# Performance work log

Hardware: AMD Instinct MI355X
Metric: run time of the kernel (lower is better)

## Reference

```python
import jax, jax.numpy as jnp
import numpy as np

B, T, E = 4, 2048, 2048
H, HKV, HD = 16, 8, 128
THETA = 10000.0
SCALE_BASE = 512.0


def _rotate_half(x):
    x1, x2 = jnp.split(x, 2, axis=-1)
    return jnp.concatenate([-x2, x1], axis=-1)


def _xpos_tables(seqlen):
    # cos/sin/scale tables for XPos rotary, all [seqlen, HD], fp32 compute dtype
    half_idx = jnp.arange(0, HD, 2, dtype=jnp.float32)
    inv_freq = 1.0 / (THETA ** (half_idx / HD))            # [HD/2]
    t = jnp.arange(seqlen, dtype=jnp.float32)
    freqs = jnp.outer(t, inv_freq)                          # [seqlen, HD/2]
    emb = jnp.concatenate([freqs, freqs], axis=-1)          # [seqlen, HD]
    cos, sin = jnp.cos(emb), jnp.sin(emb)
    # xpos decay: ((2i + 0.4d)/(1.4d)) ** ((t - L/2)/scale_base)
    scale_vec = (half_idx + 0.4 * HD) / (1.4 * HD)          # [HD/2]
    power = (t - seqlen // 2) / SCALE_BASE                  # [seqlen]
    scale = scale_vec[None, :] ** power[:, None]            # [seqlen, HD/2]
    scale = jnp.concatenate([scale, scale], axis=-1)        # [seqlen, HD]
    return cos, sin, scale


def setup_inputs() -> dict:
    key = jax.random.key(0)
    ks = jax.random.split(key, 5)
    std = 0.02
    return {
        "x": jax.random.normal(ks[0], (B, T, E), dtype=jnp.float32),
        "W_q": jax.random.normal(ks[1], (E, H * HD), dtype=jnp.float32) * std,
        "W_k": jax.random.normal(ks[2], (E, HKV * HD), dtype=jnp.float32) * std,
        "W_v": jax.random.normal(ks[3], (E, HKV * HD), dtype=jnp.float32) * std,
        "W_o": jax.random.normal(ks[4], (E, E), dtype=jnp.float32) * std,
    }


def reference(x, W_q, W_k, W_v, W_o):
    b, t, _ = x.shape
    q = (x @ W_q).reshape(b, t, H, HD)       # [B,T,H,HD]
    k = (x @ W_k).reshape(b, t, HKV, HD)     # [B,T,HKV,HD]
    v = (x @ W_v).reshape(b, t, HKV, HD)
    rep = H // HKV                            # GQA: repeat_interleave over head dim
    k = jnp.repeat(k, rep, axis=2)
    v = jnp.repeat(v, rep, axis=2)

    cos, sin, scale = _xpos_tables(t)         # past_len = 0 (no kv cache)
    cos = cos[None, :, None, :]
    sin = sin[None, :, None, :]
    scale = scale[None, :, None, :]
    q = q * scale
    q = q * cos + _rotate_half(q) * sin
    k = k / scale
    k = k * cos + _rotate_half(k) * sin

    inv_sqrt_d = 1.0 / jnp.sqrt(jnp.float32(HD))
    scores = jnp.einsum('bqhd,bkhd->bhqk', q, k) * inv_sqrt_d  # [B,H,T,T]
    causal = jnp.triu(jnp.ones((t, t), dtype=bool), k=1)
    scores = jnp.where(causal[None, None], -jnp.inf, scores)
    probs = jax.nn.softmax(scores, axis=-1)
    attn = jnp.einsum('bhqk,bkhd->bqhd', probs, v)             # [B,T,H,HD]
    out = attn.reshape(b, t, E) @ W_o
    return out
```

## Files before the change

kernel.cpp:

```cpp
#include <hip/hip_runtime.h>

typedef _Float16 f16;
typedef __attribute__((ext_vector_type(8))) _Float16 f16x8;
typedef __attribute__((ext_vector_type(4))) _Float16 f16x4;
typedef __attribute__((ext_vector_type(4))) float f32x4;
typedef __attribute__((ext_vector_type(16))) float f32x16;
typedef __attribute__((ext_vector_type(4))) unsigned u32x4;

#define T_SEQ 2048
#define NBATCH 4

__device__ __forceinline__ void gld_lds16(const f16* g, f16* l) {
    __builtin_amdgcn_global_load_lds((const __attribute__((address_space(1))) void*)g,
                                     (__attribute__((address_space(3))) void*)l, 16, 0, 0);
}

__device__ __forceinline__ unsigned pk2(float a, float b) {
    __attribute__((ext_vector_type(2))) __fp16 h = __builtin_amdgcn_cvt_pkrtz(a, b);
    return __builtin_bit_cast(unsigned, h);
}

__global__ __launch_bounds__(256) void k_prep(const float* __restrict__ x,
                                              const float* __restrict__ Wq,
                                              const float* __restrict__ Wk,
                                              const float* __restrict__ Wv,
                                              const float* __restrict__ Wo,
                                              f16* __restrict__ xh,
                                              f16* __restrict__ wqkvT,
                                              f16* __restrict__ woT,
                                              float* __restrict__ tab) {
    __shared__ float tile[32][33];
    int bidx = blockIdx.x;
    if (bidx < 16384) {
        int i = bidx * 256 + threadIdx.x;
        float4 v = ((const float4*)x)[i];
        f16x4 o = { (f16)v.x, (f16)v.y, (f16)v.z, (f16)v.w };
        ((f16x4*)xh)[i] = o;
        return;
    }
    bidx -= 16384;
    if (bidx >= 12288) {
        int i = (bidx - 12288) * 256 + threadIdx.x;
        int t = i >> 6, f = i & 63;
        float inv_freq = powf(10000.0f, -(2.0f * f) / 128.0f);
        float ang = (float)t * inv_freq;
        float sv = (2.0f * f + 51.2f) / 179.2f;
        float pw = ((float)t - 1024.0f) / 512.0f;
        tab[i] = cosf(ang);
        tab[131072 + i] = sinf(ang);
        tab[262144 + i] = powf(sv, pw);
        return;
    }
    const float* src; f16* dst; int N, bx, by;
    if (bidx < 4096)      { src = Wq; dst = wqkvT;                      N = 2048; bx = bidx & 63; by = bidx >> 6; }
    else if (bidx < 6144) { src = Wk; dst = wqkvT + (size_t)2048 * 2048; N = 1024; int t2 = bidx - 4096; bx = t2 & 31; by = t2 >> 5; }
    else if (bidx < 8192) { src = Wv; dst = wqkvT + (size_t)3072 * 2048; N = 1024; int t2 = bidx - 6144; bx = t2 & 31; by = t2 >> 5; }
    else                  { src = Wo; dst = woT;                        N = 2048; int t2 = bidx - 8192; bx = t2 & 63; by = t2 >> 6; }
    int n0 = bx * 32, k0 = by * 32;
    int tx = threadIdx.x & 31, ty = threadIdx.x >> 5;
#pragma unroll
    for (int j = 0; j < 32; j += 8)
        tile[ty + j][tx] = src[(size_t)(k0 + ty + j) * N + n0 + tx];
    __syncthreads();
#pragma unroll
    for (int j = 0; j < 32; j += 8)
        dst[(size_t)(n0 + ty + j) * 2048 + k0 + tx] = (f16)tile[tx][ty + j];
}

__global__ __launch_bounds__(256) void k_vtrans(const f16* __restrict__ qkv, f16* __restrict__ vtg) {
    const int kt = blockIdx.x, bk = blockIdx.y;
    const int b = bk >> 3, kvh = bk & 7;
    const int tid = threadIdx.x;
    __shared__ f16 tile[64][132];
#pragma unroll
    for (int p = 0; p < 4; ++p) {
        int idx = p * 256 + tid;
        int r = idx >> 4, dc = (idx & 15) * 8;
        f16x8 v = *(const f16x8*)(qkv + (size_t)(b * T_SEQ + kt * 64 + r) * 4096 + 3072 + kvh * 128 + dc);
#pragma unroll
        for (int j = 0; j < 8; ++j) tile[r][dc + j] = v[j];
    }
    __syncthreads();
    f16* outb = vtg + (size_t)(bk * 32 + kt) * 8192;
#pragma unroll
    for (int p = 0; p < 4; ++p) {
        int c = p * 256 + tid;
        int kchunk = c >> 7, d = c & 127;
        f16x8 o;
#pragma unroll
        for (int j = 0; j < 8; ++j) o[j] = tile[kchunk * 8 + j][d];
        *(f16x8*)(outb + (size_t)c * 8) = o;
    }
}

template <typename OutT>
__global__ __launch_bounds__(512, 1) void k_gemm256(const f16* __restrict__ A,
                                                    const f16* __restrict__ B,
                                                    OutT* __restrict__ C, int M, int N, int K) {
    extern __shared__ char smem[];
    f16* As = (f16*)smem;
    f16* Bs = (f16*)smem + 32768;
    const int tid = threadIdx.x, lane = tid & 63, w = tid >> 6;
    const int wr4 = w >> 1, wc2 = w & 1;
    const int cq = lane & 15, gq = lane >> 4;
    const int nbx = gridDim.x;
    const int bid0 = blockIdx.y * nbx + blockIdx.x;
    const int x = bid0 & 7, idx = bid0 >> 3;
    const int snb = (nbx == 16) ? 3 : 2;
    const int mt = (x >> 1) * 8 + (idx >> snb);
    const int nt = (x & 1) * (nbx >> 1) + (idx & ((nbx >> 1) - 1));
    const int m0 = mt * 256, n0 = nt * 256;
    const int KT = K >> 6;

    f32x4 acc[2][2][2][4] = {};
    f16x8 aL[2][2], aH[2][2], bL[4][2], bH[4][2];

    auto stageA = [&](int buf, int half, int t) {
#pragma unroll
        for (int r = 0; r < 2; ++r) {
            int cb = r * 512 + w * 64;
            int c = cb + lane;
            int row = c >> 3, cc = c & 7;
            gld_lds16(A + (size_t)(m0 + half * 128 + row) * K + t * 64 + ((cc ^ (row & 7)) * 8),
                      As + buf * 16384 + half * 8192 + cb * 8);
        }
    };
    auto stageB = [&](int buf, int half, int t) {
#pragma unroll
        for (int r = 0; r < 2; ++r) {
            int cb = r * 512 + w * 64;
            int c = cb + lane;
            int row = c >> 3, cc = c & 7;
            gld_lds16(B + (size_t)(n0 + half * 128 + row) * K + t * 64 + ((cc ^ (row & 7)) * 8),
                      Bs + buf * 16384 + half * 8192 + cb * 8);
        }
    };
    auto rdA = [&](int buf, int qr, f16x8 a[2][2]) {
#pragma unroll
        for (int mi = 0; mi < 2; ++mi)
#pragma unroll
            for (int ks = 0; ks < 2; ++ks) {
                int R = qr * 128 + wr4 * 32 + mi * 16 + cq;
                a[mi][ks] = *(const f16x8*)&As[buf * 16384 + R * 64 + (((ks * 4 + gq) ^ (cq & 7)) * 8)];
            }
    };
    auto rdB = [&](int buf, int qc, f16x8 b[4][2]) {
#pragma unroll
        for (int ni = 0; ni < 4; ++ni)
#pragma unroll
            for (int ks = 0; ks < 2; ++ks) {
                int R = qc * 128 + wc2 * 64 + ni * 16 + cq;
                b[ni][ks] = *(const f16x8*)&Bs[buf * 16384 + R * 64 + (((ks * 4 + gq) ^ (cq & 7)) * 8)];
            }
    };

    stageA(0, 0, 0); stageB(0, 0, 0); stageB(0, 1, 0); stageA(0, 1, 0);
    if (KT > 1) { stageA(1, 0, 1); stageB(1, 0, 1); stageB(1, 1, 1); }
    asm volatile("s_waitcnt vmcnt(6)");
    __builtin_amdgcn_s_barrier();

#pragma unroll 1
    for (int t = 0; t < KT; ++t) {
        const int buf = t & 1;
        rdA(buf, 0, aL); rdB(buf, 0, bL); rdB(buf, 1, bH); rdA(buf, 1, aH);
        __builtin_amdgcn_s_setprio(1);
#pragma unroll
        for (int mi = 0; mi < 2; ++mi)
#pragma unroll
            for (int ni = 0; ni < 4; ++ni)
#pragma unroll
                for (int ks = 0; ks < 2; ++ks)
                    acc[0][0][mi][ni] = __builtin_amdgcn_mfma_f32_16x16x32_f16(aL[mi][ks], bL[ni][ks], acc[0][0][mi][ni], 0, 0, 0);
        __builtin_amdgcn_s_setprio(0);
        if (t + 1 < KT) stageA(buf ^ 1, 1, t + 1);
        __builtin_amdgcn_s_setprio(1);
#pragma unroll
        for (int mi = 0; mi < 2; ++mi)
#pragma unroll
            for (int ni = 0; ni < 4; ++ni)
#pragma unroll
                for (int ks = 0; ks < 2; ++ks)
                    acc[0][1][mi][ni] = __builtin_amdgcn_mfma_f32_16x16x32_f16(aL[mi][ks], bH[ni][ks], acc[0][1][mi][ni], 0, 0, 0);
        __builtin_amdgcn_s_setprio(0);
        __builtin_amdgcn_s_barrier();
        if (t + 2 < KT) { stageA(buf, 0, t + 2); stageB(buf, 0, t + 2); stageB(buf, 1, t + 2); }
        __builtin_amdgcn_s_setprio(1);
#pragma unroll
        for (int mi = 0; mi < 2; ++mi)
#pragma unroll
            for (int ni = 0; ni < 4; ++ni)
#pragma unroll
                for (int ks = 0; ks < 2; ++ks)
                    acc[1][1][mi][ni] = __builtin_amdgcn_mfma_f32_16x16x32_f16(aH[mi][ks], bH[ni][ks], acc[1][1][mi][ni], 0, 0, 0);
#pragma unroll
        for (int mi = 0; mi < 2; ++mi)
#pragma unroll
            for (int ni = 0; ni < 4; ++ni)
#pragma unroll
                for (int ks = 0; ks < 2; ++ks)
                    acc[1][0][mi][ni] = __builtin_amdgcn_mfma_f32_16x16x32_f16(aH[mi][ks], bL[ni][ks], acc[1][0][mi][ni], 0, 0, 0);
        __builtin_amdgcn_s_setprio(0);
        if (t + 2 < KT)      asm volatile("s_waitcnt vmcnt(6)");
        else                 asm volatile("s_waitcnt vmcnt(0)");
        __builtin_amdgcn_s_barrier();
    }

#pragma unroll
    for (int qr = 0; qr < 2; ++qr)
#pragma unroll
        for (int qc = 0; qc < 2; ++qc)
#pragma unroll
            for (int mi = 0; mi < 2; ++mi)
#pragma unroll
                for (int ni = 0; ni < 4; ++ni)
#pragma unroll
                    for (int i = 0; i < 4; ++i) {
                        int row = m0 + qr * 128 + wr4 * 32 + mi * 16 + gq * 4 + i;
                        int col = n0 + qc * 128 + wc2 * 64 + ni * 16 + cq;
                        C[(size_t)row * N + col] = (OutT)acc[qr][qc][mi][ni][i];
                    }
}

__global__ __launch_bounds__(256) void k_rope(f16* __restrict__ qkv, const float* __restrict__ tab) {
    int idx = blockIdx.x * 256 + threadIdx.x;
    const int QTOT = NBATCH * T_SEQ * 16 * 64;
    int f, col0, bt;
    bool isQ = idx < QTOT;
    if (isQ) {
        f = idx & 63; int hh = (idx >> 6) & 15; bt = idx >> 10;
        col0 = hh * 128 + f;
    } else {
        int j = idx - QTOT;
        f = j & 63; int hh = (j >> 6) & 7; bt = j >> 9;
        col0 = 2048 + hh * 128 + f;
    }
    int t = bt & (T_SEQ - 1);
    float cs = tab[t * 64 + f], sn = tab[131072 + t * 64 + f], sc = tab[262144 + t * 64 + f];
    float mult = isQ ? sc * 0.08838834764831845f : 1.0f / sc;
    size_t p = (size_t)bt * 4096 + col0;
    float x1 = (float)qkv[p], x2 = (float)qkv[p + 64];
    qkv[p]      = (f16)((x1 * cs - x2 * sn) * mult);
    qkv[p + 64] = (f16)((x2 * cs + x1 * sn) * mult);
}

__global__ __launch_bounds__(512) void k_attn(const f16* __restrict__ qkv,
                                              const f16* __restrict__ vtg,
                                              f16* __restrict__ ao) {
    const int bid0 = blockIdx.x;
    const int bid = (bid0 & 7) * 32 + (bid0 >> 3);
    const int pr = bid & 7, kvh = (bid >> 3) & 7, b = bid >> 6;
    const int bk = b * 8 + kvh;
    const int tid = threadIdx.x, lane = tid & 63, w = tid >> 6;
    const int w4 = w & 3, hg = w >> 2;
    const int h = kvh * 2 + hg;
    const int l31 = lane & 31, hi = lane >> 5;

    __shared__ f16 Klds[2][64 * 128];
    __shared__ f16 Vlds[2][8 * 128 * 8];

    const f16* kbase = qkv + (size_t)b * T_SEQ * 4096 + 2048 + kvh * 128;
    const f16* vbase = vtg + (size_t)bk * 32 * 8192;

    auto stage = [&](int buf, int kt) {
#pragma unroll
        for (int qq = 0; qq < 2; ++qq) {
            int c = w * 128 + qq * 64 + lane;
            int row = c >> 4;
            int ch = (c & 15) ^ (row & 15);
            gld_lds16(kbase + (size_t)(kt * 64 + row) * 4096 + ch * 8,
                      &Klds[buf][(w * 128 + qq * 64) * 8]);
        }
#pragma unroll
        for (int qq = 0; qq < 2; ++qq) {
            int c = w * 128 + qq * 64 + lane;
            gld_lds16(vbase + ((size_t)kt * 1024 + c) * 8,
                      &Vlds[buf][(w * 128 + qq * 64) * 8]);
        }
    };

#pragma unroll 1
    for (int hf = 0; hf < 2; ++hf) {
        const int qt = hf ? pr : (15 - pr);
        const int q0 = qt * 128;
        const int nkt = 2 * qt + 2;
        const int qrow = q0 + w4 * 32 + l31;

        f16x8 qf[8];
#pragma unroll
        for (int ds = 0; ds < 8; ++ds)
            qf[ds] = *(const f16x8*)(qkv + (size_t)(b * T_SEQ + qrow) * 4096 + h * 128 + ds * 16 + hi * 8);

        f32x16 Ot[4] = {};
        float mrow = -1e30f, lrow = 0.0f;

        stage(0, 0);
        __syncthreads();

#pragma unroll 1
        for (int kt = 0; kt < nkt; ++kt) {
            const int kb = kt & 1;
            if (kt + 1 < nkt) stage(kb ^ 1, kt + 1);

            if (!(kt == 2 * qt + 1 && w4 < 2)) {
                f32x16 St0 = {}, St1 = {};
                __builtin_amdgcn_s_setprio(1);
#pragma unroll
                for (int ds = 0; ds < 8; ++ds) {
                    int slot = (((2 * ds + hi) ^ (l31 & 15)) << 3);
                    f16x8 k0 = *(const f16x8*)&Klds[kb][l31 * 128 + slot];
                    f16x8 k1 = *(const f16x8*)&Klds[kb][(32 + l31) * 128 + slot];
                    St0 = __builtin_amdgcn_mfma_f32_32x32x16_f16(k0, qf[ds], St0, 0, 0, 0);
                    St1 = __builtin_amdgcn_mfma_f32_32x32x16_f16(k1, qf[ds], St1, 0, 0, 0);
                }
                __builtin_amdgcn_s_setprio(0);

                if (kt >= 2 * qt) {
                    int kbase2 = kt * 64;
#pragma unroll
                    for (int r = 0; r < 16; ++r) {
                        int krel = (r & 3) + 8 * (r >> 2) + 4 * hi;
                        if (kbase2 + krel > qrow) St0[r] = -1e30f;
                        if (kbase2 + 32 + krel > qrow) St1[r] = -1e30f;
                    }
                }

                float tm[16];
#pragma unroll
                for (int r = 0; r < 16; ++r) tm[r] = fmaxf(St0[r], St1[r]);
#pragma unroll
                for (int d = 8; d >= 1; d >>= 1)
#pragma unroll
                    for (int r = 0; r < 8; ++r)
                        if (r < d) tm[r] = fmaxf(tm[r], tm[r + d]);
                float tmax = tm[0];
                float mtile = fmaxf(tmax, __shfl_xor(tmax, 32, 64));

                if (!__all((mtile - mrow) <= 8.0f)) {
                    float mnew = fmaxf(mrow, mtile);
                    float fs = __expf(mrow - mnew);
                    mrow = mnew;
                    lrow *= fs;
#pragma unroll
                    for (int dblk = 0; dblk < 4; ++dblk)
#pragma unroll
                        for (int e = 0; e < 16; ++e) Ot[dblk][e] *= fs;
                }
#pragma unroll
                for (int r = 0; r < 16; ++r) {
                    St0[r] = __expf(St0[r] - mrow);
                    St1[r] = __expf(St1[r] - mrow);
                }
                float ts[16];
#pragma unroll
                for (int r = 0; r < 16; ++r) ts[r] = St0[r] + St1[r];
#pragma unroll
                for (int d = 8; d >= 1; d >>= 1)
#pragma unroll
                    for (int r = 0; r < 8; ++r)
                        if (r < d) ts[r] += ts[r + d];
                float tsum = ts[0];
                lrow += tsum + __shfl_xor(tsum, 32, 64);

#define PV_P(o, pos) ((o) < 4 ? St0[((o) & 3) * 4 + (pos)] : St1[((o) & 3) * 4 + (pos)])
#pragma unroll
                for (int s = 0; s < 4; ++s) {
                    unsigned x1 = pk2(PV_P(2 * s, 0), PV_P(2 * s, 1));
                    unsigned x2 = pk2(PV_P(2 * s, 2), PV_P(2 * s, 3));
                    unsigned y1 = pk2(PV_P(2 * s + 1, 0), PV_P(2 * s + 1, 1));
                    unsigned y2 = pk2(PV_P(2 * s + 1, 2), PV_P(2 * s + 1, 3));
                    unsigned sx1 = __shfl_xor(x1, 32, 64);
                    unsigned sx2 = __shfl_xor(x2, 32, 64);
                    unsigned sy1 = __shfl_xor(y1, 32, 64);
                    unsigned sy2 = __shfl_xor(y2, 32, 64);
                    u32x4 pw;
                    pw[0] = hi ? sy1 : x1;
                    pw[1] = hi ? sy2 : x2;
                    pw[2] = hi ? y1 : sx1;
                    pw[3] = hi ? y2 : sx2;
                    f16x8 pa = __builtin_bit_cast(f16x8, pw);
                    __builtin_amdgcn_s_setprio(1);
#pragma unroll
                    for (int dblk = 0; dblk < 4; ++dblk) {
                        f16x8 vb = *(const f16x8*)&Vlds[kb][(((2 * s + hi) << 7) + 32 * dblk + l31) << 3];
                        Ot[dblk] = __builtin_amdgcn_mfma_f32_32x32x16_f16(vb, pa, Ot[dblk], 0, 0, 0);
                    }
                    __builtin_amdgcn_s_setprio(0);
                }
#undef PV_P
            }
            __syncthreads();
        }

        {
            float inv = 1.0f / lrow;
            size_t rowb = (size_t)(b * T_SEQ + qrow) * 2048 + h * 128;
#pragma unroll
            for (int dblk = 0; dblk < 4; ++dblk)
#pragma unroll
                for (int rg = 0; rg < 4; ++rg) {
                    f16x4 o4 = { (f16)(Ot[dblk][rg * 4 + 0] * inv), (f16)(Ot[dblk][rg * 4 + 1] * inv),
                                 (f16)(Ot[dblk][rg * 4 + 2] * inv), (f16)(Ot[dblk][rg * 4 + 3] * inv) };
                    *(f16x4*)(ao + rowb + dblk * 32 + rg * 8 + hi * 4) = o4;
                }
        }
    }
}

extern "C" void kernel_launch(void* const* d_in, const int* in_sizes, int n_in,
                              void* d_out, int out_size, void* d_ws, size_t ws_size,
                              hipStream_t stream) {
    const float* x  = (const float*)d_in[0];
    const float* Wq = (const float*)d_in[1];
    const float* Wk = (const float*)d_in[2];
    const float* Wv = (const float*)d_in[3];
    const float* Wo = (const float*)d_in[4];
    float* out = (float*)d_out;

    f16* xh    = (f16*)d_ws;
    f16* wqkvT = xh + (size_t)16777216;
    f16* woT   = wqkvT + (size_t)8388608;
    f16* qkv   = woT + (size_t)4194304;
    float* tab = (float*)(qkv + (size_t)33554432);
    f16* ao  = xh;
    f16* vtg = wqkvT;

    hipFuncSetAttribute(reinterpret_cast<const void*>(&k_gemm256<f16>),
                        hipFuncAttributeMaxDynamicSharedMemorySize, 131072);
    hipFuncSetAttribute(reinterpret_cast<const void*>(&k_gemm256<float>),
                        hipFuncAttributeMaxDynamicSharedMemorySize, 131072);

    k_prep<<<29184, 256, 0, stream>>>(x, Wq, Wk, Wv, Wo, xh, wqkvT, woT, tab);
    k_gemm256<f16><<<dim3(16, 32), 512, 131072, stream>>>(xh, wqkvT, qkv, 8192, 4096, 2048);
    k_vtrans<<<dim3(32, 32), 256, 0, stream>>>(qkv, vtg);
    k_rope<<<49152, 256, 0, stream>>>(qkv, tab);
    k_attn<<<256, 512, 0, stream>>>(qkv, vtg, ao);
    k_gemm256<float><<<dim3(8, 32), 512, 131072, stream>>>(ao, woT, out, 8192, 2048, 2048);
}
```

Before: 373.7 us.

## Triple-buffer K/V tiles in attention with explicit vmcnt waits

Moves the attention kernel's K/V shared buffers to dynamic LDS with three stages instead of two. Loads are issued two tiles ahead, and each iteration waits with a counted s_waitcnt vmcnt plus a raw s_barrier instead of a full __syncthreads. This is meant to hide more global-load latency behind the MFMA work. In exchange it uses 96KB of LDS and depends on hand-counted outstanding loads (4 per stage), which is fragile if the compiler emits other vector memory ops inside the loop.

```diff
diff --git a/kernel.cpp b/kernel.cpp
--- a/kernel.cpp
+++ b/kernel.cpp
@@ -246,6 +246,7 @@
 __global__ __launch_bounds__(512) void k_attn(const f16* __restrict__ qkv,
                                               const f16* __restrict__ vtg,
                                               f16* __restrict__ ao) {
+    extern __shared__ f16 asmem[];
     const int bid0 = blockIdx.x;
     const int bid = (bid0 & 7) * 32 + (bid0 >> 3);
     const int pr = bid & 7, kvh = (bid >> 3) & 7, b = bid >> 6;
@@ -255,26 +256,23 @@
     const int h = kvh * 2 + hg;
     const int l31 = lane & 31, hi = lane >> 5;
 
-    __shared__ f16 Klds[2][64 * 128];
-    __shared__ f16 Vlds[2][8 * 128 * 8];
-
     const f16* kbase = qkv + (size_t)b * T_SEQ * 4096 + 2048 + kvh * 128;
     const f16* vbase = vtg + (size_t)bk * 32 * 8192;
 
     auto stage = [&](int buf, int kt) {
+        f16* kb_ = asmem + buf * 16384;
+        f16* vb_ = kb_ + 8192;
 #pragma unroll
         for (int qq = 0; qq < 2; ++qq) {
             int c = w * 128 + qq * 64 + lane;
             int row = c >> 4;
             int ch = (c & 15) ^ (row & 15);
-            gld_lds16(kbase + (size_t)(kt * 64 + row) * 4096 + ch * 8,
-                      &Klds[buf][(w * 128 + qq * 64) * 8]);
+            gld_lds16(kbase + (size_t)(kt * 64 + row) * 4096 + ch * 8, kb_ + (w * 128 + qq * 64) * 8);
         }
 #pragma unroll
         for (int qq = 0; qq < 2; ++qq) {
             int c = w * 128 + qq * 64 + lane;
-            gld_lds16(vbase + ((size_t)kt * 1024 + c) * 8,
-                      &Vlds[buf][(w * 128 + qq * 64) * 8]);
+            gld_lds16(vbase + ((size_t)kt * 1024 + c) * 8, vb_ + (w * 128 + qq * 64) * 8);
         }
     };
 
@@ -294,12 +292,16 @@
         float mrow = -1e30f, lrow = 0.0f;
 
         stage(0, 0);
-        __syncthreads();
+        if (nkt > 1) stage(1, 1);
 
 #pragma unroll 1
         for (int kt = 0; kt < nkt; ++kt) {
-            const int kb = kt & 1;
-            if (kt + 1 < nkt) stage(kb ^ 1, kt + 1);
+            const int kb = kt % 3;
+            const f16* Kl = asmem + kb * 16384;
+            const f16* Vl = Kl + 8192;
+            if (kt + 1 < nkt) asm volatile("s_waitcnt vmcnt(4)");
+            else              asm volatile("s_waitcnt vmcnt(0)");
+            __builtin_amdgcn_s_barrier();
 
             if (!(kt == 2 * qt + 1 && w4 < 2)) {
                 f32x16 St0 = {}, St1 = {};
@@ -307,8 +309,8 @@
 #pragma unroll
                 for (int ds = 0; ds < 8; ++ds) {
                     int slot = (((2 * ds + hi) ^ (l31 & 15)) << 3);
-                    f16x8 k0 = *(const f16x8*)&Klds[kb][l31 * 128 + slot];
-                    f16x8 k1 = *(const f16x8*)&Klds[kb][(32 + l31) * 128 + slot];
+                    f16x8 k0 = *(const f16x8*)&Kl[l31 * 128 + slot];
+                    f16x8 k1 = *(const f16x8*)&Kl[(32 + l31) * 128 + slot];
                     St0 = __builtin_amdgcn_mfma_f32_32x32x16_f16(k0, qf[ds], St0, 0, 0, 0);
                     St1 = __builtin_amdgcn_mfma_f32_32x32x16_f16(k1, qf[ds], St1, 0, 0, 0);
                 }
@@ -381,14 +383,15 @@
                     __builtin_amdgcn_s_setprio(1);
 #pragma unroll
                     for (int dblk = 0; dblk < 4; ++dblk) {
-                        f16x8 vb = *(const f16x8*)&Vlds[kb][(((2 * s + hi) << 7) + 32 * dblk + l31) << 3];
+                        f16x8 vb = *(const f16x8*)&Vl[(((2 * s + hi) << 7) + 32 * dblk + l31) << 3];
                         Ot[dblk] = __builtin_amdgcn_mfma_f32_32x32x16_f16(vb, pa, Ot[dblk], 0, 0, 0);
                     }
                     __builtin_amdgcn_s_setprio(0);
                 }
 #undef PV_P
             }
-            __syncthreads();
+            __builtin_amdgcn_s_barrier();
+            if (kt + 2 < nkt) stage((kt + 2) % 3, kt + 2);
         }
 
         {
@@ -428,11 +431,13 @@
                         hipFuncAttributeMaxDynamicSharedMemorySize, 131072);
     hipFuncSetAttribute(reinterpret_cast<const void*>(&k_gemm256<float>),
                         hipFuncAttributeMaxDynamicSharedMemorySize, 131072);
+    hipFuncSetAttribute(reinterpret_cast<const void*>(&k_attn),
+                        hipFuncAttributeMaxDynamicSharedMemorySize, 98304);
 
     k_prep<<<29184, 256, 0, stream>>>(x, Wq, Wk, Wv, Wo, xh, wqkvT, woT, tab);
     k_gemm256<f16><<<dim3(16, 32), 512, 131072, stream>>>(xh, wqkvT, qkv, 8192, 4096, 2048);
     k_vtrans<<<dim3(32, 32), 256, 0, stream>>>(qkv, vtg);
     k_rope<<<49152, 256, 0, stream>>>(qkv, tab);
-    k_attn<<<256, 512, 0, stream>>>(qkv, vtg, ao);
+    k_attn<<<256, 512, 98304, stream>>>(qkv, vtg, ao);
     k_gemm256<float><<<dim3(8, 32), 512, 131072, stream>>>(ao, woT, out, 8192, 2048, 2048);
 }
```

Measured after the change: 370.5 us. About the same (-0.9%).
